# Kernel tuning notes

Measured on AMD Instinct MI355X. Metric: run time of the kernel, lower is better.

Reference implementation:

```python
import jax, jax.numpy as jnp
import numpy as np

B, V, NF, K = 16, 5000, 352, 120


def setup_inputs() -> dict:
    key = jax.random.key(0)
    k1, k2, k3, k4 = jax.random.split(key, 4)
    return {
        "feat_x": jax.random.normal(k1, (B, V, NF), dtype=jnp.float32),
        "feat_y": jax.random.normal(k2, (B, V, NF), dtype=jnp.float32),
        "evecs_x": jax.random.normal(k3, (B, V, K), dtype=jnp.float32),
        "evecs_y": jax.random.normal(k4, (B, V, K), dtype=jnp.float32),
    }


def reference(feat_x, feat_y, evecs_x, evecs_y):
    # Spectral coefficients: F_hat[b] = (evecs_x[b]^T feat_x[b])^T -> [B, F, K]
    F_hat = jnp.einsum("bvk,bvf->bfk", evecs_x, feat_x)
    G_hat = jnp.einsum("bvk,bvf->bfk", evecs_y, feat_y)

    # C1[b] = (inv(F^T F) F^T G)^T, batched least-squares solve
    FtF = jnp.einsum("bfk,bfl->bkl", F_hat, F_hat)  # [B,K,K]
    FtG = jnp.einsum("bfk,bfl->bkl", F_hat, G_hat)  # [B,K,K]
    C1 = jnp.linalg.solve(FtF, FtG).transpose(0, 2, 1)

    GtG = jnp.einsum("bfk,bfl->bkl", G_hat, G_hat)
    GtF = jnp.einsum("bfk,bfl->bkl", G_hat, F_hat)
    C2 = jnp.linalg.solve(GtG, GtF).transpose(0, 2, 1)
    return (C1, C2)
```

## Files before the change

kernel.cpp:

```cpp
#include <hip/hip_runtime.h>
#include <hip/hip_bf16.h>

#define NB 16
#define VV 5000
#define NFD 352
#define KD 120
#define NCH 5
#define SLABSZ (352 * 120)

typedef __attribute__((ext_vector_type(8))) short short8;
typedef __attribute__((ext_vector_type(4))) float float4v;

__device__ __forceinline__ unsigned short bfb(float a) {
    return __builtin_bit_cast(unsigned short, __float2bfloat16(a));
}

__device__ __forceinline__ void pack8(const float* f, int4& hi, int4& lo) {
    unsigned short h[8], l[8];
    #pragma unroll
    for (int j = 0; j < 8; ++j) {
        const float a = f[j];
        const __hip_bfloat16 hb = __float2bfloat16(a);
        h[j] = __builtin_bit_cast(unsigned short, hb);
        l[j] = bfb(a - __bfloat162float(hb));
    }
    hi.x = h[0] | (h[1] << 16); hi.y = h[2] | (h[3] << 16);
    hi.z = h[4] | (h[5] << 16); hi.w = h[6] | (h[7] << 16);
    lo.x = l[0] | (l[1] << 16); lo.y = l[2] | (l[3] << 16);
    lo.z = l[4] | (l[5] << 16); lo.w = l[6] | (l[7] << 16);
}

__global__ __launch_bounds__(256, 2) void proj_mfma(
    const float* __restrict__ fx, const float* __restrict__ fy,
    const float* __restrict__ ex, const float* __restrict__ ey,
    float* __restrict__ partials)
{
    const int t = threadIdx.x;

    int lin = blockIdx.x + 15 * (blockIdx.y + 2 * blockIdx.z);
    lin = (lin & 7) * 60 + (lin >> 3);
    const int xx   = lin % 15;
    const int rest = lin / 15;
    const int wh = rest & 1;
    const int b  = rest >> 1;
    const int mt = xx % 3;
    const int ch = xx / 3;

    const float* Ab = (wh ? fy : fx) + (size_t)b * VV * NFD;
    const float* Bb = (wh ? ey : ex) + (size_t)b * VV * KD;
    const int m0 = mt * 128;

    __shared__ int4 smem4[4096];
    unsigned char* smem = (unsigned char*)smem4;

    int acol[2], awb[2], ao[2];
    #pragma unroll
    for (int i = 0; i < 2; ++i) {
        const int q = i * 256 + t;
        const int m = q & 127;
        const int o = q >> 7;
        acol[i] = min(m0 + m, NFD - 1);
        awb[i]  = m * 64 + ((o ^ ((m >> 1) & 3)) * 16);
        ao[i]   = o;
    }
    int bcol[2], bwb[2], bo[2];
    #pragma unroll
    for (int i = 0; i < 2; ++i) {
        const int q = i * 256 + t;
        const int n = q & 127;
        const int o = q >> 7;
        bcol[i] = min(n, KD - 1);
        bwb[i]  = n * 64 + ((o ^ ((n >> 1) & 3)) * 16);
        bo[i]   = o;
    }

    const int lane = t & 63;
    const int wid  = t >> 6;
    const int wm = wid >> 1, wn = wid & 1;
    const int r16 = lane & 15;
    const int g   = lane >> 4;

    int abase[4], bbase[4];
    #pragma unroll
    for (int mf = 0; mf < 4; ++mf) {
        const int m = wm * 64 + mf * 16 + r16;
        abase[mf] = m * 64 + ((g ^ ((m >> 1) & 3)) * 16);
    }
    #pragma unroll
    for (int nf = 0; nf < 4; ++nf) {
        const int n = wn * 64 + nf * 16 + r16;
        bbase[nf] = n * 64 + ((g ^ ((n >> 1) & 3)) * 16);
    }

    float4v acc[4][4];
    #pragma unroll
    for (int mf = 0; mf < 4; ++mf)
        #pragma unroll
        for (int nf = 0; nf < 4; ++nf)
            acc[mf][nf] = float4v{0.f, 0.f, 0.f, 0.f};

    const int step0 = ch * 32;
    const int nst   = (ch < 4) ? 32 : 30;

    float faP[2][8], fbP[2][8], faQ[2][8], fbQ[2][8];

    auto do_loads = [&](int st, float (&fa)[2][8], float (&fb)[2][8]) {
        const int v0 = (step0 + st) * 32;
        if (v0 + 32 <= VV) {
            #pragma unroll
            for (int i = 0; i < 2; ++i) {
                const float* pa = Ab + (size_t)(v0 + ao[i] * 8) * NFD + acol[i];
                #pragma unroll
                for (int j = 0; j < 8; ++j) fa[i][j] = pa[j * NFD];
            }
            #pragma unroll
            for (int i = 0; i < 2; ++i) {
                const float* pb = Bb + (size_t)(v0 + bo[i] * 8) * KD + bcol[i];
                #pragma unroll
                for (int j = 0; j < 8; ++j) fb[i][j] = pb[j * KD];
            }
        } else {
            #pragma unroll
            for (int i = 0; i < 2; ++i) {
                const float* pa = Ab + (size_t)(v0 + ao[i] * 8) * NFD + acol[i];
                #pragma unroll
                for (int j = 0; j < 8; ++j) {
                    const int v = v0 + ao[i] * 8 + j;
                    fa[i][j] = (v < VV) ? pa[j * NFD] : 0.f;
                }
            }
            #pragma unroll
            for (int i = 0; i < 2; ++i) {
                const float* pb = Bb + (size_t)(v0 + bo[i] * 8) * KD + bcol[i];
                #pragma unroll
                for (int j = 0; j < 8; ++j) {
                    const int v = v0 + bo[i] * 8 + j;
                    fb[i][j] = (v < VV) ? pb[j * KD] : 0.f;
                }
            }
        }
    };

    auto do_writes = [&](int bufb, float (&fa)[2][8], float (&fb)[2][8]) {
        #pragma unroll
        for (int i = 0; i < 2; ++i) {
            int4 hi, lo;
            pack8(fa[i], hi, lo);
            *(int4*)(smem + bufb + awb[i])        = hi;
            *(int4*)(smem + bufb + awb[i] + 8192) = lo;
        }
        #pragma unroll
        for (int i = 0; i < 2; ++i) {
            int4 hi, lo;
            pack8(fb[i], hi, lo);
            *(int4*)(smem + bufb + 16384 + bwb[i]) = hi;
            *(int4*)(smem + bufb + 24576 + bwb[i]) = lo;
        }
    };

    auto compute = [&](int bufb) {
        short8 ah[4], al[4], bh[4], bl[4];
        #pragma unroll
        for (int mf = 0; mf < 4; ++mf) {
            ah[mf] = *(const short8*)(smem + bufb + abase[mf]);
            al[mf] = *(const short8*)(smem + bufb + abase[mf] + 8192);
        }
        #pragma unroll
        for (int nf = 0; nf < 4; ++nf) {
            bh[nf] = *(const short8*)(smem + bufb + 16384 + bbase[nf]);
            bl[nf] = *(const short8*)(smem + bufb + 24576 + bbase[nf]);
        }
        #pragma unroll
        for (int mf = 0; mf < 4; ++mf)
            #pragma unroll
            for (int nf = 0; nf < 4; ++nf) {
                acc[mf][nf] = __builtin_amdgcn_mfma_f32_16x16x32_bf16(ah[mf], bh[nf], acc[mf][nf], 0, 0, 0);
                acc[mf][nf] = __builtin_amdgcn_mfma_f32_16x16x32_bf16(ah[mf], bl[nf], acc[mf][nf], 0, 0, 0);
                acc[mf][nf] = __builtin_amdgcn_mfma_f32_16x16x32_bf16(al[mf], bh[nf], acc[mf][nf], 0, 0, 0);
            }
    };

    do_loads(0, faP, fbP);
    do_loads(1, faQ, fbQ);
    do_writes(0, faP, fbP);
    __syncthreads();

    for (int i = 0; i < nst / 2; ++i) {
        const int st = 2 * i;
        if (st + 2 < nst) do_loads(st + 2, faP, fbP);
        compute(0);
        do_writes(32768, faQ, fbQ);
        __syncthreads();
        if (st + 3 < nst) do_loads(st + 3, faQ, fbQ);
        compute(32768);
        if (st + 2 < nst) do_writes(0, faP, fbP);
        __syncthreads();
    }

    float* slab = partials + (size_t)((ch * 2 + wh) * NB + b) * SLABSZ;
    #pragma unroll
    for (int mf = 0; mf < 4; ++mf) {
        const int mrow = mt * 128 + wm * 64 + mf * 16 + g * 4;
        #pragma unroll
        for (int nf = 0; nf < 4; ++nf) {
            const int n = wn * 64 + nf * 16 + r16;
            if (n < KD) {
                #pragma unroll
                for (int r = 0; r < 4; ++r) {
                    const int m = mrow + r;
                    if (m < NFD) slab[(size_t)m * KD + n] = acc[mf][nf][r];
                }
            }
        }
    }
}

__global__ __launch_bounds__(256) void reduce_k(
    const float* __restrict__ partials, float* __restrict__ fhat, float* __restrict__ ghat)
{
    const int id = blockIdx.x * 256 + threadIdx.x;
    if (id >= NFD * KD) return;
    const int wb = blockIdx.y;
    const int wh = wb >> 4;
    const int b  = wb & 15;

    const float* p = partials + (size_t)(wh * NB + b) * SLABSZ + id;
    const size_t chstride = (size_t)2 * NB * SLABSZ;

    float s = 0.f;
    #pragma unroll
    for (int c = 0; c < NCH; ++c) s += p[c * chstride];

    float* dst = (wh ? ghat : fhat) + (size_t)b * NFD * KD + id;
    *dst = s;
}

__device__ __forceinline__ void gemm_tn_64x64(
    const float* __restrict__ A, const float* __restrict__ B, float* __restrict__ C,
    int V, int M, int N, int m0, int n0)
{
    __shared__ float As[16][64];
    __shared__ float Bs[16][64];

    const int tid = threadIdx.x;
    const int tx = tid & 15;
    const int ty = tid >> 4;
    const int sr = tid >> 4;
    const int sc = (tid & 15) << 2;

    float acc[4][4] = {{0.f,0.f,0.f,0.f},{0.f,0.f,0.f,0.f},
                       {0.f,0.f,0.f,0.f},{0.f,0.f,0.f,0.f}};

    for (int v0 = 0; v0 < V; v0 += 16) {
        const int v = v0 + sr;
        float4 av; av.x = av.y = av.z = av.w = 0.f;
        float4 bv; bv.x = bv.y = bv.z = bv.w = 0.f;
        if (v < V) {
            const float* Ar = A + (size_t)v * M;
            const int ca = m0 + sc;
            if (ca + 3 < M) {
                av = *(const float4*)(Ar + ca);
            } else {
                if (ca + 0 < M) av.x = Ar[ca + 0];
                if (ca + 1 < M) av.y = Ar[ca + 1];
                if (ca + 2 < M) av.z = Ar[ca + 2];
                if (ca + 3 < M) av.w = Ar[ca + 3];
            }
            const float* Br = B + (size_t)v * N;
            const int cb = n0 + sc;
            if (cb + 3 < N) {
                bv = *(const float4*)(Br + cb);
            } else {
                if (cb + 0 < N) bv.x = Br[cb + 0];
                if (cb + 1 < N) bv.y = Br[cb + 1];
                if (cb + 2 < N) bv.z = Br[cb + 2];
                if (cb + 3 < N) bv.w = Br[cb + 3];
            }
        }
        __syncthreads();
        *(float4*)&As[sr][sc] = av;
        *(float4*)&Bs[sr][sc] = bv;
        __syncthreads();

        #pragma unroll
        for (int kk = 0; kk < 16; ++kk) {
            const float4 a4 = *(const float4*)&As[kk][ty << 2];
            const float4 b4 = *(const float4*)&Bs[kk][tx << 2];
            const float a[4]  = {a4.x, a4.y, a4.z, a4.w};
            const float bb[4] = {b4.x, b4.y, b4.z, b4.w};
            #pragma unroll
            for (int i = 0; i < 4; ++i)
                #pragma unroll
                for (int j = 0; j < 4; ++j)
                    acc[i][j] = fmaf(a[i], bb[j], acc[i][j]);
        }
    }

    #pragma unroll
    for (int i = 0; i < 4; ++i) {
        const int m = m0 + (ty << 2) + i;
        if (m < M) {
            #pragma unroll
            for (int j = 0; j < 4; ++j) {
                const int n = n0 + (tx << 2) + j;
                if (n < N) C[(size_t)m * N + n] = acc[i][j];
            }
        }
    }
}

__global__ __launch_bounds__(256) void gram_kernel(
    const float* __restrict__ fhat, const float* __restrict__ ghat,
    float* __restrict__ ftf, float* __restrict__ gtg, float* __restrict__ ftg)
{
    const int b = blockIdx.z;
    const int which = blockIdx.y;
    const int m0 = (blockIdx.x & 1) * 64;
    const int n0 = (blockIdx.x >> 1) * 64;

    const float* F = fhat + (size_t)b * NFD * KD;
    const float* G = ghat + (size_t)b * NFD * KD;
    const float* A  = (which == 1) ? G : F;
    const float* Bp = (which == 0) ? F : G;
    float* C = ((which == 0) ? ftf : (which == 1) ? gtg : ftg) + (size_t)b * KD * KD;

    gemm_tn_64x64(A, Bp, C, NFD, KD, KD, m0, n0);
}

__device__ __forceinline__ float ldval(const float* __restrict__ A, const float* __restrict__ B,
                                       int pair, int row, int col) {
    if (col < KD) return A[row * KD + col];
    const int l = col - KD;
    return pair ? B[l * KD + row] : B[row * KD + l];
}

#define FOR15(OP) OP(0) OP(1) OP(2) OP(3) OP(4) OP(5) OP(6) OP(7) OP(8) OP(9) \
                  OP(10) OP(11) OP(12) OP(13) OP(14)

__global__ __launch_bounds__(480, 1) void solve_kernel(
    const float* __restrict__ ftf, const float* __restrict__ gtg,
    const float* __restrict__ ftg, float* __restrict__ out)
{
    const int pair = blockIdx.x;
    const int b = blockIdx.y;
    const int tid = threadIdx.x;
    const int cg = tid & 15;
    const int rg = tid >> 4;
    const int cbase = cg * 15;
    const int r0 = rg * 4;
    const int seg = cg * 20;

    const float* Ag = ((pair == 0) ? ftf : gtg) + (size_t)b * KD * KD;
    const float* Bg = ftg + (size_t)b * KD * KD;

    __shared__ __align__(16) float prow[2][320];
    __shared__ __align__(16) float pcol[2][120];

    #define DECL(I) float w##I = ldval(Ag, Bg, pair, r0 + 0, cbase + (I)); \
                    float x##I = ldval(Ag, Bg, pair, r0 + 1, cbase + (I)); \
                    float y##I = ldval(Ag, Bg, pair, r0 + 2, cbase + (I)); \
                    float z##I = ldval(Ag, Bg, pair, r0 + 3, cbase + (I));
    FOR15(DECL)
    #undef DECL

    if (rg == 0) {
        #define PUB0(I) prow[0][seg + (I)] = w##I;
        FOR15(PUB0)
        #undef PUB0
    }
    if (cg == 0) *(float4*)&pcol[0][r0] = float4{w0, x0, y0, z0};
    __syncthreads();

    int jseg = 0, joff = 0;

    for (int j = 0; j < KD; ++j) {
        const int cur = j & 1;
        const int nxt = cur ^ 1;

        const float pinv = 1.0f / prow[cur][jseg * 20 + joff];
        const float4 f4 = *(const float4*)&pcol[cur][r0];

        const float4 q0 = *(const float4*)&prow[cur][seg + 0];
        const float4 q1 = *(const float4*)&prow[cur][seg + 4];
        const float4 q2 = *(const float4*)&prow[cur][seg + 8];
        const float4 q3 = *(const float4*)&prow[cur][seg + 12];
        const float p0 = q0.x, p1 = q0.y, p2 = q0.z, p3 = q0.w;
        const float p4 = q1.x, p5 = q1.y, p6 = q1.z, p7 = q1.w;
        const float p8 = q2.x, p9 = q2.y, p10 = q2.z, p11 = q2.w;
        const float p12 = q3.x, p13 = q3.y, p14 = q3.z;

        const float fw = f4.x * pinv, fx = f4.y * pinv;
        const float fy = f4.z * pinv, fz = f4.w * pinv;

        #define UPD(I) w##I = fmaf(-fw, p##I, w##I); x##I = fmaf(-fx, p##I, x##I); \
                       y##I = fmaf(-fy, p##I, y##I); z##I = fmaf(-fz, p##I, z##I);
        FOR15(UPD)
        #undef UPD

        if (rg == (j >> 2)) {
            #define FW(I) w##I = p##I * pinv;
            #define FX(I) x##I = p##I * pinv;
            #define FY(I) y##I = p##I * pinv;
            #define FZ(I) z##I = p##I * pinv;
            switch (j & 3) {
                case 0: FOR15(FW) break;
                case 1: FOR15(FX) break;
                case 2: FOR15(FY) break;
                default: FOR15(FZ) break;
            }
            #undef FW
            #undef FX
            #undef FY
            #undef FZ
        }

        const int j2 = j + 1;

        if (j2 < KD && rg == (j2 >> 2)) {
            #define PW(I) prow[nxt][seg + (I)] = w##I;
            #define PX(I) prow[nxt][seg + (I)] = x##I;
            #define PY(I) prow[nxt][seg + (I)] = y##I;
            #define PZ(I) prow[nxt][seg + (I)] = z##I;
            switch (j2 & 3) {
                case 0: FOR15(PW) break;
                case 1: FOR15(PX) break;
                case 2: FOR15(PY) break;
                default: FOR15(PZ) break;
            }
            #undef PW
            #undef PX
            #undef PY
            #undef PZ
        }

        joff++; if (joff == 15) { joff = 0; jseg++; }
        if (j2 < KD && cg == jseg) {
            #define PC(I) case I: *(float4*)&pcol[nxt][r0] = float4{w##I, x##I, y##I, z##I}; break;
            switch (joff) {
                FOR15(PC)
                default: break;
            }
            #undef PC
        }
        __syncthreads();
    }

    if (cg >= 8) {
        float* op = out + (size_t)pair * NB * KD * KD + (size_t)b * KD * KD;
        #define OUTW(I) { const int l = cbase + (I) - KD; \
                          *(float4*)&op[l * KD + r0] = float4{w##I, x##I, y##I, z##I}; }
        FOR15(OUTW)
        #undef OUTW
    }
}

extern "C" void kernel_launch(void* const* d_in, const int* in_sizes, int n_in,
                              void* d_out, int out_size, void* d_ws, size_t ws_size,
                              hipStream_t stream)
{
    const float* feat_x  = (const float*)d_in[0];
    const float* feat_y  = (const float*)d_in[1];
    const float* evecs_x = (const float*)d_in[2];
    const float* evecs_y = (const float*)d_in[3];
    float* out = (float*)d_out;

    float* ws       = (float*)d_ws;
    float* partials = ws;
    float* fhat     = partials + (size_t)NCH * 2 * NB * SLABSZ;
    float* ghat     = fhat + (size_t)NB * NFD * KD;
    float* ftf      = ws;
    float* gtg      = ftf + (size_t)NB * KD * KD;
    float* ftg      = gtg + (size_t)NB * KD * KD;

    proj_mfma <<<dim3(15, 2, NB), 256, 0, stream>>>(feat_x, feat_y, evecs_x, evecs_y, partials);
    reduce_k  <<<dim3(165, 32), 256, 0, stream>>>(partials, fhat, ghat);
    gram_kernel<<<dim3(4, 3, NB), 256, 0, stream>>>(fhat, ghat, ftf, gtg, ftg);
    solve_kernel<<<dim3(2, NB), 480, 0, stream>>>(ftf, gtg, ftg, out);
}
```

Baseline: 208.8 us.

## Load MFMA operands directly from global into registers, dropping LDS staging

Removes the shared-memory double buffer and the block-wide barriers. Each wave now loads its own A and B fragment columns straight from global memory into registers, splits them into bf16 hi/lo and feeds the MFMAs. The intent is to eliminate LDS writes and reads plus the sync stalls. In exchange, A and B strips are fetched redundantly by two waves each, global accesses become less coalesced (16 contiguous floats per row group), and register pressure rises with the 4x8 prefetch arrays, which may hurt occupancy.

```diff
diff --git a/kernel.cpp b/kernel.cpp
--- a/kernel.cpp
+++ b/kernel.cpp
@@ -50,47 +50,20 @@
     const float* Bb = (wh ? ey : ex) + (size_t)b * VV * KD;
     const int m0 = mt * 128;
 
-    __shared__ int4 smem4[4096];
-    unsigned char* smem = (unsigned char*)smem4;
-
-    int acol[2], awb[2], ao[2];
-    #pragma unroll
-    for (int i = 0; i < 2; ++i) {
-        const int q = i * 256 + t;
-        const int m = q & 127;
-        const int o = q >> 7;
-        acol[i] = min(m0 + m, NFD - 1);
-        awb[i]  = m * 64 + ((o ^ ((m >> 1) & 3)) * 16);
-        ao[i]   = o;
-    }
-    int bcol[2], bwb[2], bo[2];
-    #pragma unroll
-    for (int i = 0; i < 2; ++i) {
-        const int q = i * 256 + t;
-        const int n = q & 127;
-        const int o = q >> 7;
-        bcol[i] = min(n, KD - 1);
-        bwb[i]  = n * 64 + ((o ^ ((n >> 1) & 3)) * 16);
-        bo[i]   = o;
-    }
-
     const int lane = t & 63;
     const int wid  = t >> 6;
     const int wm = wid >> 1, wn = wid & 1;
     const int r16 = lane & 15;
     const int g   = lane >> 4;
-
-    int abase[4], bbase[4];
-    #pragma unroll
-    for (int mf = 0; mf < 4; ++mf) {
-        const int m = wm * 64 + mf * 16 + r16;
-        abase[mf] = m * 64 + ((g ^ ((m >> 1) & 3)) * 16);
-    }
-    #pragma unroll
-    for (int nf = 0; nf < 4; ++nf) {
-        const int n = wn * 64 + nf * 16 + r16;
-        bbase[nf] = n * 64 + ((g ^ ((n >> 1) & 3)) * 16);
-    }
+    const int vbase = g * 8;
+
+    int acolw[4], bcolw[4];
+    #pragma unroll
+    for (int mf = 0; mf < 4; ++mf)
+        acolw[mf] = min(m0 + wm * 64 + mf * 16 + r16, NFD - 1);
+    #pragma unroll
+    for (int nf = 0; nf < 4; ++nf)
+        bcolw[nf] = min(wn * 64 + nf * 16 + r16, KD - 1);
 
     float4v acc[4][4];
     #pragma unroll
@@ -99,76 +72,62 @@
         for (int nf = 0; nf < 4; ++nf)
             acc[mf][nf] = float4v{0.f, 0.f, 0.f, 0.f};
 
-    const int step0 = ch * 32;
-    const int nst   = (ch < 4) ? 32 : 30;
-
-    float faP[2][8], fbP[2][8], faQ[2][8], fbQ[2][8];
-
-    auto do_loads = [&](int st, float (&fa)[2][8], float (&fb)[2][8]) {
-        const int v0 = (step0 + st) * 32;
-        if (v0 + 32 <= VV) {
-            #pragma unroll
-            for (int i = 0; i < 2; ++i) {
-                const float* pa = Ab + (size_t)(v0 + ao[i] * 8) * NFD + acol[i];
-                #pragma unroll
-                for (int j = 0; j < 8; ++j) fa[i][j] = pa[j * NFD];
-            }
-            #pragma unroll
-            for (int i = 0; i < 2; ++i) {
-                const float* pb = Bb + (size_t)(v0 + bo[i] * 8) * KD + bcol[i];
-                #pragma unroll
-                for (int j = 0; j < 8; ++j) fb[i][j] = pb[j * KD];
-            }
+    const int chv0 = ch * 1024;
+    const int nst  = (ch < 4) ? 32 : 29;
+    const bool lastch = (ch == 4);
+
+    float faP[4][8], fbP[4][8], faQ[4][8], fbQ[4][8];
+
+    auto do_load = [&](float (&fa)[4][8], float (&fb)[4][8], int st, bool tail) {
+        const int v0 = chv0 + st * 32 + vbase;
+        const float* pa = Ab + (size_t)v0 * NFD;
+        const float* pb = Bb + (size_t)v0 * KD;
+        if (!tail) {
+            #pragma unroll
+            for (int mf = 0; mf < 4; ++mf)
+                #pragma unroll
+                for (int j = 0; j < 8; ++j)
+                    fa[mf][j] = pa[j * NFD + acolw[mf]];
+            #pragma unroll
+            for (int nf = 0; nf < 4; ++nf)
+                #pragma unroll
+                for (int j = 0; j < 8; ++j)
+                    fb[nf][j] = pb[j * KD + bcolw[nf]];
         } else {
             #pragma unroll
-            for (int i = 0; i < 2; ++i) {
-                const float* pa = Ab + (size_t)(v0 + ao[i] * 8) * NFD + acol[i];
-                #pragma unroll
-                for (int j = 0; j < 8; ++j) {
-                    const int v = v0 + ao[i] * 8 + j;
-                    fa[i][j] = (v < VV) ? pa[j * NFD] : 0.f;
+            for (int j = 0; j < 8; ++j) {
+                const bool ok = (v0 + j) < VV;
+                #pragma unroll
+                for (int mf = 0; mf < 4; ++mf) {
+                    float v = 0.f;
+                    if (ok) v = pa[j * NFD + acolw[mf]];
+                    fa[mf][j] = v;
                 }
-            }
-            #pragma unroll
-            for (int i = 0; i < 2; ++i) {
-                const float* pb = Bb + (size_t)(v0 + bo[i] * 8) * KD + bcol[i];
-                #pragma unroll
-                for (int j = 0; j < 8; ++j) {
-                    const int v = v0 + bo[i] * 8 + j;
-                    fb[i][j] = (v < VV) ? pb[j * KD] : 0.f;
+                #pragma unroll
+                for (int nf = 0; nf < 4; ++nf) {
+                    float v = 0.f;
+                    if (ok) v = pb[j * KD + bcolw[nf]];
+                    fb[nf][j] = v;
                 }
             }
         }
     };
 
-    auto do_writes = [&](int bufb, float (&fa)[2][8], float (&fb)[2][8]) {
-        #pragma unroll
-        for (int i = 0; i < 2; ++i) {
+    auto do_compute = [&](float (&fa)[4][8], float (&fb)[4][8]) {
+        short8 ah[4], al[4], bh[4], bl[4];
+        #pragma unroll
+        for (int mf = 0; mf < 4; ++mf) {
             int4 hi, lo;
-            pack8(fa[i], hi, lo);
-            *(int4*)(smem + bufb + awb[i])        = hi;
-            *(int4*)(smem + bufb + awb[i] + 8192) = lo;
-        }
-        #pragma unroll
-        for (int i = 0; i < 2; ++i) {
+            pack8(fa[mf], hi, lo);
+            ah[mf] = __builtin_bit_cast(short8, hi);
+            al[mf] = __builtin_bit_cast(short8, lo);
+        }
+        #pragma unroll
+        for (int nf = 0; nf < 4; ++nf) {
             int4 hi, lo;
-            pack8(fb[i], hi, lo);
-            *(int4*)(smem + bufb + 16384 + bwb[i]) = hi;
-            *(int4*)(smem + bufb + 24576 + bwb[i]) = lo;
-        }
-    };
-
-    auto compute = [&](int bufb) {
-        short8 ah[4], al[4], bh[4], bl[4];
-        #pragma unroll
-        for (int mf = 0; mf < 4; ++mf) {
-            ah[mf] = *(const short8*)(smem + bufb + abase[mf]);
-            al[mf] = *(const short8*)(smem + bufb + abase[mf] + 8192);
-        }
-        #pragma unroll
-        for (int nf = 0; nf < 4; ++nf) {
-            bh[nf] = *(const short8*)(smem + bufb + 16384 + bbase[nf]);
-            bl[nf] = *(const short8*)(smem + bufb + 24576 + bbase[nf]);
+            pack8(fb[nf], hi, lo);
+            bh[nf] = __builtin_bit_cast(short8, hi);
+            bl[nf] = __builtin_bit_cast(short8, lo);
         }
         #pragma unroll
         for (int mf = 0; mf < 4; ++mf)
@@ -180,21 +139,13 @@
             }
     };
 
-    do_loads(0, faP, fbP);
-    do_loads(1, faQ, fbQ);
-    do_writes(0, faP, fbP);
-    __syncthreads();
-
-    for (int i = 0; i < nst / 2; ++i) {
-        const int st = 2 * i;
-        if (st + 2 < nst) do_loads(st + 2, faP, fbP);
-        compute(0);
-        do_writes(32768, faQ, fbQ);
-        __syncthreads();
-        if (st + 3 < nst) do_loads(st + 3, faQ, fbQ);
-        compute(32768);
-        if (st + 2 < nst) do_writes(0, faP, fbP);
-        __syncthreads();
+    do_load(faP, fbP, 0, lastch && (nst == 1));
+    for (int st = 0; st < nst; st += 2) {
+        if (st + 1 < nst) do_load(faQ, fbQ, st + 1, lastch && (st + 1 == nst - 1));
+        do_compute(faP, fbP);
+        if (st + 1 >= nst) break;
+        if (st + 2 < nst) do_load(faP, fbP, st + 2, lastch && (st + 2 == nst - 1));
+        do_compute(faQ, fbQ);
     }
 
     float* slab = partials + (size_t)((ch * 2 + wh) * NB + b) * SLABSZ;
```

New measurement: 279.4 us. +33.8%, slower.
